# Kernel tuning notes

Hardware: AMD Instinct MI355X
Metric: run time of the kernel (lower is better)

The kernel has to match this reference:

```python
import jax, jax.numpy as jnp
import numpy as np

PH, PW = 7, 7
SPATIAL_SCALE = 0.0625


def _hat_int(t):
    # Antiderivative of the unit hat (triangle) function phi(t)=max(0,1-|t|),
    # i.e. integral_{-inf}^{t} phi. Piecewise quadratic, saturates to [0,1].
    t = jnp.clip(t, -1.0, 1.0)
    return jnp.where(t <= 0, 0.5 * (t + 1.0) ** 2, 1.0 - 0.5 * (1.0 - t) ** 2)


def _bin_weights(lo, hi, size):
    # lo, hi: [R, P] continuous bin boundaries (in feature-map coordinates).
    # Returns [R, P, size]: exact 1D integral of the hat basis at each integer
    # grid node over [lo, hi]. Bilinear interpolation is the tensor product of
    # 1D hat bases, so the exact 2D PrRoI integral separates into these weights.
    grid = jnp.arange(size, dtype=lo.dtype)
    return _hat_int(hi[..., None] - grid) - _hat_int(lo[..., None] - grid)


def _prroi_pool(features, rois):
    N, C, H, W = features.shape
    R = rois.shape[0]
    dt = features.dtype
    bidx = rois[:, 0].astype(jnp.int32)
    x1 = rois[:, 1] * SPATIAL_SCALE
    y1 = rois[:, 2] * SPATIAL_SCALE
    x2 = rois[:, 3] * SPATIAL_SCALE
    y2 = rois[:, 4] * SPATIAL_SCALE
    roi_w = jnp.maximum(x2 - x1, 0.0)
    roi_h = jnp.maximum(y2 - y1, 0.0)
    bw = roi_w / PW  # [R]
    bh = roi_h / PH
    px = jnp.arange(PW, dtype=dt)
    py = jnp.arange(PH, dtype=dt)
    x_lo = x1[:, None] + px[None, :] * bw[:, None]  # [R, PW]
    x_hi = x_lo + bw[:, None]
    y_lo = y1[:, None] + py[None, :] * bh[:, None]  # [R, PH]
    y_hi = y_lo + bh[:, None]
    Wx = _bin_weights(x_lo, x_hi, W)  # [R, PW, W]
    Wy = _bin_weights(y_lo, y_hi, H)  # [R, PH, H]
    area = bw * bh  # [R]
    inv_area = jnp.where(area > 0, 1.0 / jnp.maximum(area, 1e-12), 0.0)
    out = jnp.zeros((R, C, PH, PW), dtype=dt)
    for n in range(N):  # small fixed batch loop; avoids [R,C,H,W] gather
        m = (bidx == n).astype(dt)
        out = out + jnp.einsum('rph,chw,rqw->rcpq', Wy * m[:, None, None], features[n], Wx)
    return out * inv_area[:, None, None, None]


def setup_inputs() -> dict:
    key = jax.random.key(0)
    k1, k2, k3, k4, k5, k6 = jax.random.split(key, 6)
    N, C, H, W, R = 2, 256, 152, 152, 512
    features = jax.random.normal(k1, (N, C, H, W), dtype=jnp.float32)
    img = H / SPATIAL_SCALE  # 2432 px image
    bidx = jax.random.randint(k2, (R,), 0, N).astype(jnp.float32)
    x1 = jax.random.uniform(k3, (R,), minval=0.0, maxval=img * 0.7)
    y1 = jax.random.uniform(k4, (R,), minval=0.0, maxval=img * 0.7)
    x2 = x1 + jax.random.uniform(k5, (R,), minval=32.0, maxval=img * 0.3)
    y2 = y1 + jax.random.uniform(k6, (R,), minval=32.0, maxval=img * 0.3)
    rois = jnp.stack([bidx, x1, y1, x2, y2], axis=1).astype(jnp.float32)
    return {"features": features, "rois": rois}


def reference(features, rois):
    return _prroi_pool(features, rois)
```

## Files before the change

kernel.cpp:

```cpp
#include <hip/hip_runtime.h>

#define PHH 7
#define PWW 7
static constexpr float SPATIAL_SCALE = 0.0625f;

__device__ __forceinline__ float hat_int(float t) {
    t = fminf(fmaxf(t, -1.0f), 1.0f);
    float a = t + 1.0f, b = 1.0f - t;
    return (t <= 0.0f) ? 0.5f * a * a : 1.0f - 0.5f * b * b;
}

__device__ __forceinline__ float bin_w(float lo, float hi, float g) {
    return hat_int(hi - g) - hat_int(lo - g);
}

__device__ __forceinline__ unsigned short f32_to_bf16_rne(float x) {
    unsigned int u = __float_as_uint(x);
    unsigned int r = 0x7FFFu + ((u >> 16) & 1u);
    return (unsigned short)((u + r) >> 16);
}

__device__ __forceinline__ float bf_lo(unsigned int v) {
    return __uint_as_float(v << 16);
}
__device__ __forceinline__ float bf_hi(unsigned int v) {
    return __uint_as_float(v & 0xFFFF0000u);
}

__global__ __launch_bounds__(256) void transpose_nchw_nhwc_bf16(
    const float* __restrict__ src, unsigned short* __restrict__ dst, int C, int HW)
{
    __shared__ float tile[32][33];
    const int n = blockIdx.z;
    const int hw0 = blockIdx.x * 32;
    const int c0 = blockIdx.y * 32;
    const float* s = src + (size_t)n * C * HW;
    unsigned short* d = dst + (size_t)n * C * HW;
    const int tx = threadIdx.x, ty = threadIdx.y;
    #pragma unroll
    for (int i = ty; i < 32; i += 8) {
        int c = c0 + i, hw = hw0 + tx;
        if (c < C && hw < HW) tile[i][tx] = s[(size_t)c * HW + hw];
    }
    __syncthreads();
    #pragma unroll
    for (int i = ty; i < 32; i += 8) {
        int hw = hw0 + i, c = c0 + tx;
        if (c < C && hw < HW) d[(size_t)hw * C + c] = f32_to_bf16_rne(tile[tx][i]);
    }
}

__global__ __launch_bounds__(256) void prroi_pool_p4(
    const unsigned short* __restrict__ ft,
    const float* __restrict__ rois,
    float* __restrict__ out,
    int H, int W, int R)
{
    const int nwg = R * PHH;
    int task = (int)blockIdx.x;
    if ((nwg & 7) == 0) {
        const int chunk = nwg >> 3;
        task = (task & 7) * chunk + (task >> 3);
    }
    const int r = task / PHH;
    const int p = task % PHH;

    const int tid = threadIdx.x;
    const int wig = tid >> 6;
    const int lane = tid & 63;
    const int c = lane * 4;

    const float* roi = rois + (size_t)r * 5;
    const int b = (int)roi[0];
    const float x1 = roi[1] * SPATIAL_SCALE;
    const float y1 = roi[2] * SPATIAL_SCALE;
    const float x2 = roi[3] * SPATIAL_SCALE;
    const float y2 = roi[4] * SPATIAL_SCALE;
    const float bw = fmaxf(x2 - x1, 0.0f) / (float)PWW;
    const float bh = fmaxf(y2 - y1, 0.0f) / (float)PHH;
    const float area = bw * bh;
    const float inv_area = (area > 0.0f) ? 1.0f / fmaxf(area, 1e-12f) : 0.0f;

    const float ylo = y1 + (float)p * bh;
    const float yhi = ylo + bh;
    const int h0 = max(0, (int)ceilf(ylo - 1.0f));
    const int h1 = min(H - 1, (int)floorf(yhi + 1.0f));
    const int w0 = max(0, (int)ceilf(x1 - 1.0f));
    const int w1 = min(W - 1, (int)floorf(x2 + 1.0f));
    const int nh = min(h1 - h0 + 1, 16);
    const int ww = w1 - w0 + 1;

    __shared__ float wx8[152 * 8];
    __shared__ float wys[16];
    __shared__ float rbuf[64 * 29];

    const int wwpad = (ww + 7) & ~7;
    for (int i = tid; i < wwpad; i += 256) {
        const float g = (float)(w0 + i);
        #pragma unroll
        for (int q = 0; q < PWW; ++q) {
            const float lo = x1 + (float)q * bw;
            wx8[i * 8 + q] = (i < ww) ? bin_w(lo, lo + bw, g) : 0.0f;
        }
        wx8[i * 8 + 7] = 0.0f;
    }
    for (int i = tid; i < nh; i += 256)
        wys[i] = bin_w(ylo, yhi, (float)(h0 + i));
    __syncthreads();

    float acc[PWW][4];
    #pragma unroll
    for (int q = 0; q < PWW; ++q)
        #pragma unroll
        for (int ch = 0; ch < 4; ++ch) acc[q][ch] = 0.0f;

    const size_t rowstride = (size_t)W * 256;
    const unsigned short* base =
        ft + ((size_t)b * H + (size_t)h0) * rowstride + (size_t)w0 * 256 + c;

    for (int chunk = 0; chunk < ww; chunk += 8) {
        int off[8];
        #pragma unroll
        for (int j = 0; j < 8; ++j)
            off[j] = (chunk + j < ww) ? (chunk + j) * 256 : 0;

        float u[4][8];
        #pragma unroll
        for (int ch = 0; ch < 4; ++ch)
            #pragma unroll
            for (int j = 0; j < 8; ++j) u[ch][j] = 0.0f;

        int i = wig;
        for (; i + 4 < nh; i += 8) {
            const unsigned short* rp0 = base + (size_t)i * rowstride;
            const unsigned short* rp1 = base + (size_t)(i + 4) * rowstride;
            uint2 v0[8], v1[8];
            #pragma unroll
            for (int j = 0; j < 8; ++j) v0[j] = *(const uint2*)(rp0 + off[j]);
            #pragma unroll
            for (int j = 0; j < 8; ++j) v1[j] = *(const uint2*)(rp1 + off[j]);
            const float wy0 = wys[i];
            const float wy1 = wys[i + 4];
            #pragma unroll
            for (int j = 0; j < 8; ++j) {
                u[0][j] = fmaf(wy0, bf_lo(v0[j].x), u[0][j]);
                u[1][j] = fmaf(wy0, bf_hi(v0[j].x), u[1][j]);
                u[2][j] = fmaf(wy0, bf_lo(v0[j].y), u[2][j]);
                u[3][j] = fmaf(wy0, bf_hi(v0[j].y), u[3][j]);
            }
            #pragma unroll
            for (int j = 0; j < 8; ++j) {
                u[0][j] = fmaf(wy1, bf_lo(v1[j].x), u[0][j]);
                u[1][j] = fmaf(wy1, bf_hi(v1[j].x), u[1][j]);
                u[2][j] = fmaf(wy1, bf_lo(v1[j].y), u[2][j]);
                u[3][j] = fmaf(wy1, bf_hi(v1[j].y), u[3][j]);
            }
        }
        for (; i < nh; i += 4) {
            const unsigned short* rp0 = base + (size_t)i * rowstride;
            uint2 v0[8];
            #pragma unroll
            for (int j = 0; j < 8; ++j) v0[j] = *(const uint2*)(rp0 + off[j]);
            const float wy0 = wys[i];
            #pragma unroll
            for (int j = 0; j < 8; ++j) {
                u[0][j] = fmaf(wy0, bf_lo(v0[j].x), u[0][j]);
                u[1][j] = fmaf(wy0, bf_hi(v0[j].x), u[1][j]);
                u[2][j] = fmaf(wy0, bf_lo(v0[j].y), u[2][j]);
                u[3][j] = fmaf(wy0, bf_hi(v0[j].y), u[3][j]);
            }
        }

        #pragma unroll
        for (int j = 0; j < 8; ++j) {
            const float4 wa = *(const float4*)&wx8[(chunk + j) * 8];
            const float4 wb = *(const float4*)&wx8[(chunk + j) * 8 + 4];
            #pragma unroll
            for (int ch = 0; ch < 4; ++ch) {
                acc[0][ch] = fmaf(wa.x, u[ch][j], acc[0][ch]);
                acc[1][ch] = fmaf(wa.y, u[ch][j], acc[1][ch]);
                acc[2][ch] = fmaf(wa.z, u[ch][j], acc[2][ch]);
                acc[3][ch] = fmaf(wa.w, u[ch][j], acc[3][ch]);
                acc[4][ch] = fmaf(wb.x, u[ch][j], acc[4][ch]);
                acc[5][ch] = fmaf(wb.y, u[ch][j], acc[5][ch]);
                acc[6][ch] = fmaf(wb.z, u[ch][j], acc[6][ch]);
            }
        }
    }

    for (int g = 1; g < 4; ++g) {
        if (wig == g) {
            #pragma unroll
            for (int q = 0; q < PWW; ++q)
                #pragma unroll
                for (int ch = 0; ch < 4; ++ch)
                    rbuf[lane * 29 + q * 4 + ch] = acc[q][ch];
        }
        __syncthreads();
        if (wig == 0) {
            #pragma unroll
            for (int q = 0; q < PWW; ++q)
                #pragma unroll
                for (int ch = 0; ch < 4; ++ch)
                    acc[q][ch] += rbuf[lane * 29 + q * 4 + ch];
        }
        __syncthreads();
    }

    if (wig == 0) {
        float* o = out + ((size_t)r * 256 + c) * (PHH * PWW) + p * PWW;
        #pragma unroll
        for (int ch = 0; ch < 4; ++ch)
            #pragma unroll
            for (int q = 0; q < PWW; ++q)
                o[(size_t)ch * (PHH * PWW) + q] = acc[q][ch] * inv_area;
    }
}

__global__ __launch_bounds__(256) void prroi_pool_nchw(
    const float* __restrict__ f, const float* __restrict__ rois,
    float* __restrict__ out, int C, int H, int W, int R)
{
    const int idx = blockIdx.x * blockDim.x + threadIdx.x;
    const int total = R * C * PHH * PWW;
    if (idx >= total) return;
    const int q = idx % PWW;
    const int p = (idx / PWW) % PHH;
    const int c = (idx / (PWW * PHH)) % C;
    const int r = idx / (PWW * PHH * C);
    const float* roi = rois + (size_t)r * 5;
    const int b = (int)roi[0];
    const float x1 = roi[1] * SPATIAL_SCALE;
    const float y1 = roi[2] * SPATIAL_SCALE;
    const float x2 = roi[3] * SPATIAL_SCALE;
    const float y2 = roi[4] * SPATIAL_SCALE;
    const float bw = fmaxf(x2 - x1, 0.0f) / (float)PWW;
    const float bh = fmaxf(y2 - y1, 0.0f) / (float)PHH;
    const float area = bw * bh;
    const float inv_area = (area > 0.0f) ? 1.0f / fmaxf(area, 1e-12f) : 0.0f;
    const float xlo = x1 + (float)q * bw, xhi = xlo + bw;
    const float ylo = y1 + (float)p * bh, yhi = ylo + bh;
    const int h0 = max(0, (int)ceilf(ylo - 1.0f));
    const int h1 = min(H - 1, (int)floorf(yhi + 1.0f));
    const int w0 = max(0, (int)ceilf(xlo - 1.0f));
    const int w1 = min(W - 1, (int)floorf(xhi + 1.0f));
    float acc = 0.0f;
    for (int h = h0; h <= h1; ++h) {
        const float wy = bin_w(ylo, yhi, (float)h);
        const float* fr = f + (((size_t)b * C + c) * H + h) * W;
        for (int w = w0; w <= w1; ++w)
            acc = fmaf(wy * bin_w(xlo, xhi, (float)w), fr[w], acc);
    }
    out[idx] = acc * inv_area;
}

extern "C" void kernel_launch(void* const* d_in, const int* in_sizes, int n_in,
                              void* d_out, int out_size, void* d_ws, size_t ws_size,
                              hipStream_t stream)
{
    const float* features = (const float*)d_in[0];
    const float* rois = (const float*)d_in[1];
    float* out = (float*)d_out;

    const int C = 256, H = 152, W = 152;
    const int N = in_sizes[0] / (C * H * W);
    const int R = in_sizes[1] / 5;

    const size_t need = (size_t)N * C * H * W * sizeof(unsigned short);
    if (ws_size >= need && C == 256) {
        unsigned short* ft = (unsigned short*)d_ws;
        const int HW = H * W;
        dim3 tgrid((HW + 31) / 32, (C + 31) / 32, N);
        transpose_nchw_nhwc_bf16<<<tgrid, dim3(32, 8), 0, stream>>>(features, ft, C, HW);
        prroi_pool_p4<<<R * PHH, 256, 0, stream>>>(ft, rois, out, H, W, R);
    } else {
        const int total = R * C * PHH * PWW;
        prroi_pool_nchw<<<(total + 255) / 256, 256, 0, stream>>>(features, rois, out, C, H, W, R);
    }
}
```

Measured before the change: 69.79 us.

## Split column chunks across waves and reduce partials in one shared-memory pass

The four waves in a block now each take a separate strided set of 8-column chunks and walk every row, where before each wave took a subset of rows and all waves walked every column chunk. The serial three-step reduction into wave 0 is replaced by every wave writing its partials to a larger shared buffer, then all 256 threads each summing one channel and writing it out. This cuts barrier count, lets all threads share the final store, and may balance work better for wide ROIs. It costs more shared memory, which may lower occupancy, and waves go idle when the ROI has few column chunks.

```diff
diff --git a/kernel.cpp b/kernel.cpp
--- a/kernel.cpp
+++ b/kernel.cpp
@@ -50,7 +50,7 @@
     }
 }
 
-__global__ __launch_bounds__(256) void prroi_pool_p4(
+__global__ __launch_bounds__(256) void prroi_pool_cs(
     const unsigned short* __restrict__ ft,
     const float* __restrict__ rois,
     float* __restrict__ out,
@@ -59,8 +59,8 @@
     const int nwg = R * PHH;
     int task = (int)blockIdx.x;
     if ((nwg & 7) == 0) {
-        const int chunk = nwg >> 3;
-        task = (task & 7) * chunk + (task >> 3);
+        const int cpx = nwg >> 3;
+        task = (task & 7) * cpx + (task >> 3);
     }
     const int r = task / PHH;
     const int p = task % PHH;
@@ -68,7 +68,7 @@
     const int tid = threadIdx.x;
     const int wig = tid >> 6;
     const int lane = tid & 63;
-    const int c = lane * 4;
+    const int c0 = lane * 4;
 
     const float* roi = rois + (size_t)r * 5;
     const int b = (int)roi[0];
@@ -89,12 +89,12 @@
     const int w1 = min(W - 1, (int)floorf(x2 + 1.0f));
     const int nh = min(h1 - h0 + 1, 16);
     const int ww = w1 - w0 + 1;
+    const int wwpad = (ww + 7) & ~7;
 
     __shared__ float wx8[152 * 8];
     __shared__ float wys[16];
-    __shared__ float rbuf[64 * 29];
-
-    const int wwpad = (ww + 7) & ~7;
+    __shared__ float rbuf[4 * 64 * 29];
+
     for (int i = tid; i < wwpad; i += 256) {
         const float g = (float)(w0 + i);
         #pragma unroll
@@ -116,9 +116,9 @@
 
     const size_t rowstride = (size_t)W * 256;
     const unsigned short* base =
-        ft + ((size_t)b * H + (size_t)h0) * rowstride + (size_t)w0 * 256 + c;
-
-    for (int chunk = 0; chunk < ww; chunk += 8) {
+        ft + ((size_t)b * H + (size_t)h0) * rowstride + (size_t)w0 * 256 + c0;
+
+    for (int chunk = wig * 8; chunk < ww; chunk += 32) {
         int off[8];
         #pragma unroll
         for (int j = 0; j < 8; ++j)
@@ -130,17 +130,17 @@
             #pragma unroll
             for (int j = 0; j < 8; ++j) u[ch][j] = 0.0f;
 
-        int i = wig;
-        for (; i + 4 < nh; i += 8) {
+        int i = 0;
+        for (; i + 1 < nh; i += 2) {
             const unsigned short* rp0 = base + (size_t)i * rowstride;
-            const unsigned short* rp1 = base + (size_t)(i + 4) * rowstride;
+            const unsigned short* rp1 = rp0 + rowstride;
             uint2 v0[8], v1[8];
             #pragma unroll
             for (int j = 0; j < 8; ++j) v0[j] = *(const uint2*)(rp0 + off[j]);
             #pragma unroll
             for (int j = 0; j < 8; ++j) v1[j] = *(const uint2*)(rp1 + off[j]);
             const float wy0 = wys[i];
-            const float wy1 = wys[i + 4];
+            const float wy1 = wys[i + 1];
             #pragma unroll
             for (int j = 0; j < 8; ++j) {
                 u[0][j] = fmaf(wy0, bf_lo(v0[j].x), u[0][j]);
@@ -156,7 +156,7 @@
                 u[3][j] = fmaf(wy1, bf_hi(v1[j].y), u[3][j]);
             }
         }
-        for (; i < nh; i += 4) {
+        if (i < nh) {
             const unsigned short* rp0 = base + (size_t)i * rowstride;
             uint2 v0[8];
             #pragma unroll
@@ -188,32 +188,25 @@
         }
     }
 
-    for (int g = 1; g < 4; ++g) {
-        if (wig == g) {
-            #pragma unroll
-            for (int q = 0; q < PWW; ++q)
-                #pragma unroll
-                for (int ch = 0; ch < 4; ++ch)
-                    rbuf[lane * 29 + q * 4 + ch] = acc[q][ch];
-        }
-        __syncthreads();
-        if (wig == 0) {
-            #pragma unroll
-            for (int q = 0; q < PWW; ++q)
-                #pragma unroll
-                for (int ch = 0; ch < 4; ++ch)
-                    acc[q][ch] += rbuf[lane * 29 + q * 4 + ch];
-        }
-        __syncthreads();
-    }
-
-    if (wig == 0) {
-        float* o = out + ((size_t)r * 256 + c) * (PHH * PWW) + p * PWW;
+    #pragma unroll
+    for (int q = 0; q < PWW; ++q)
         #pragma unroll
         for (int ch = 0; ch < 4; ++ch)
-            #pragma unroll
-            for (int q = 0; q < PWW; ++q)
-                o[(size_t)ch * (PHH * PWW) + q] = acc[q][ch] * inv_area;
+            rbuf[wig * (64 * 29) + lane * 29 + q * 4 + ch] = acc[q][ch];
+    __syncthreads();
+
+    {
+        const int cc = tid;
+        const int lsrc = (cc >> 2) * 29 + (cc & 3);
+        float* o = out + ((size_t)r * 256 + cc) * (PHH * PWW) + p * PWW;
+        #pragma unroll
+        for (int q = 0; q < PWW; ++q) {
+            const float s = rbuf[lsrc + q * 4]
+                          + rbuf[1 * (64 * 29) + lsrc + q * 4]
+                          + rbuf[2 * (64 * 29) + lsrc + q * 4]
+                          + rbuf[3 * (64 * 29) + lsrc + q * 4];
+            o[q] = s * inv_area;
+        }
     }
 }
 
@@ -272,7 +265,7 @@
         const int HW = H * W;
         dim3 tgrid((HW + 31) / 32, (C + 31) / 32, N);
         transpose_nchw_nhwc_bf16<<<tgrid, dim3(32, 8), 0, stream>>>(features, ft, C, HW);
-        prroi_pool_p4<<<R * PHH, 256, 0, stream>>>(ft, rois, out, H, W, R);
+        prroi_pool_cs<<<R * PHH, 256, 0, stream>>>(ft, rois, out, H, W, R);
     } else {
         const int total = R * C * PHH * PWW;
         prroi_pool_nchw<<<(total + 255) / 256, 256, 0, stream>>>(features, rois, out, C, H, W, R);
```

After: 60.06 us. 1.16x faster.
